# Kernel tuning notes

Measured on AMD Instinct MI355X. Metric: run time of the kernel, lower is better.

The kernel has to match this reference:

```python
import jax, jax.numpy as jnp
import numpy as np
from jax import lax

# Paraformer-large streaming decoder dims
L, H, DFF, NH, DK, K, V, T, S, CKV, LB = 16, 512, 2048, 4, 128, 11, 8404, 64, 2048, 256, 256


def _ln(x, g, b, eps=1e-5):
    m = jnp.mean(x, axis=-1, keepdims=True)
    var = jnp.mean((x - m) ** 2, axis=-1, keepdims=True)
    return (x - m) * lax.rsqrt(var + eps) * g + b


def setup_inputs() -> dict:
    key = jax.random.key(0)
    ks = jax.random.split(key, 20)
    w = lambda k, shp: jax.random.normal(k, shp, jnp.float32) * 0.02
    return {
        "encoder_out": jax.random.normal(ks[0], (1, S, H), jnp.float32),
        "list_frame": jax.random.normal(ks[1], (1, T, H), jnp.float32),
        "fsmn_cache": jax.random.normal(ks[2], (L, 1, H, K - 1), jnp.float32),
        "key_cache": jax.random.normal(ks[3], (L, NH, DK, CKV), jnp.float32),
        "value_cache": jax.random.normal(ks[4], (L, NH, CKV, DK), jnp.float32),
        "norm1_g": jnp.ones((L, H)), "norm1_b": jnp.zeros((L, H)),
        "norm2_g": jnp.ones((L, H)), "norm2_b": jnp.zeros((L, H)),
        "norm3_g": jnp.ones((L, H)), "norm3_b": jnp.zeros((L, H)),
        "ffn_norm_g": jnp.ones((L, DFF)), "ffn_norm_b": jnp.zeros((L, DFF)),
        "w1": w(ks[5], (L, H, DFF)), "b1": jnp.zeros((L, DFF)),
        "w2": w(ks[6], (L, DFF, H)),  # bias-free in FunASR DecoderSANM
        "fsmn_w": w(ks[7], (L, H, K)),  # depthwise conv, groups=H, no bias
        "qw": w(ks[8], (L, H, H)), "qb": jnp.zeros((L, H)),
        "kvw": w(ks[9], (L, H, 2 * H)), "kvb": jnp.zeros((L, 2 * H)),
        "ow": w(ks[10], (L, H, H)), "ob": jnp.zeros((L, H)),
        "d3_norm1_g": jnp.ones((H,)), "d3_norm1_b": jnp.zeros((H,)),
        "d3_w1": w(ks[11], (H, DFF)), "d3_b1": jnp.zeros((DFF,)),
        "d3_ffn_norm_g": jnp.ones((DFF,)), "d3_ffn_norm_b": jnp.zeros((DFF,)),
        "d3_w2": w(ks[12], (DFF, H)),
        "after_norm_g": jnp.ones((H,)), "after_norm_b": jnp.zeros((H,)),
        "out_w": w(ks[13], (H, V)), "out_b": jnp.zeros((V,)),
        "list_frame_len": T,
    }


def reference(encoder_out, list_frame, fsmn_cache, key_cache, value_cache,
              norm1_g, norm1_b, norm2_g, norm2_b, norm3_g, norm3_b,
              ffn_norm_g, ffn_norm_b, w1, b1, w2, fsmn_w, qw, qb, kvw, kvb, ow, ob,
              d3_norm1_g, d3_norm1_b, d3_w1, d3_b1, d3_ffn_norm_g, d3_ffn_norm_b, d3_w2,
              after_norm_g, after_norm_b, out_w, out_b, list_frame_len):
    enc = encoder_out[0]  # [S, H]
    scale = DK ** -0.5

    def layer_fn(lf, p):
        (fc, kc, vc, n1g, n1b, n2g, n2b, n3g, n3b, fng, fnb,
         W1, B1, W2, FW, QW, QB, KVW, KVB, OW, OB) = p
        residual = lf
        y = _ln(lf, n1g, n1b)
        y = _ln(jax.nn.relu(y @ W1 + B1), fng, fnb) @ W2
        y = _ln(y, n2g, n2b)
        # cache concat; slice [look_back:] with look_back = -(K-1)-T keeps all K-1+T cols
        x_cat = jnp.concatenate([fc, jnp.swapaxes(y, 1, 2)], axis=-1)  # [1, H, K-1+T]
        conv = lax.conv_general_dilated(
            x_cat, FW[:, None, :], (1,), 'VALID',
            dimension_numbers=('NCH', 'OIH', 'NCH'), feature_group_count=H)  # [1, H, T]
        x = jnp.swapaxes(conv, 1, 2) + y + residual
        residual = x
        q = (_ln(x, n3g, n3b)[0] @ QW + QB).reshape(-1, NH, DK).transpose(1, 0, 2) * scale  # [h, T, dk]
        kv = enc @ KVW + KVB  # [S, 2H]
        k = kv[:, :H].reshape(-1, NH, DK).transpose(1, 2, 0)  # [h, dk, S]
        v = kv[:, H:].reshape(-1, NH, DK).transpose(1, 0, 2)  # [h, S, dk]
        k = jnp.concatenate([kc, k], axis=2)  # [h, dk, CKV+S]
        v = jnp.concatenate([vc, v], axis=1)  # [h, CKV+S, dk]
        attn = jax.nn.softmax(jnp.einsum('htd,hds->hts', q, k), axis=-1)
        ctx = jnp.einsum('hts,hsd->htd', attn, v).transpose(1, 0, 2).reshape(1, -1, H)
        lf = residual + ctx @ OW + OB
        return lf, (x_cat, k[:, :, -LB:], v[:, -LB:, :])

    layer_params = (fsmn_cache, key_cache, value_cache, norm1_g, norm1_b, norm2_g, norm2_b,
                    norm3_g, norm3_b, ffn_norm_g, ffn_norm_b, w1, b1, w2, fsmn_w,
                    qw, qb, kvw, kvb, ow, ob)
    lf, (save_fsmn, save_keys, save_values) = lax.scan(layer_fn, list_frame, layer_params)
    x = _ln(lf, d3_norm1_g, d3_norm1_b)
    x = _ln(jax.nn.relu(x @ d3_w1 + d3_b1), d3_ffn_norm_g, d3_ffn_norm_b) @ d3_w2
    logits = _ln(x, after_norm_g, after_norm_b) @ out_w + out_b
    max_logit_ids = jnp.argmax(logits, axis=-1).astype(jnp.int32)
    return save_fsmn, save_keys, save_values, max_logit_ids
```

## Files before the change

### kernel.cpp

```cpp
#include <hip/hip_runtime.h>

constexpr int LAY = 16, HID = 512, FF = 2048, NHD = 4, DKH = 128, KW = 11,
              VOC = 8404, TT = 64, SEQ = 2048, LBN = 256;

__global__ void diag_k(float* __restrict__ p, float v) { p[threadIdx.x] = v; }

__global__ __launch_bounds__(256) void copy_k(const float* __restrict__ in,
                                              float* __restrict__ out, int n) {
  const int i = blockIdx.x * 256 + threadIdx.x;
  if (i < n) out[i] = in[i];
}

__global__ __launch_bounds__(256) void ln_k(const float* __restrict__ src,
                                            const float* __restrict__ g,
                                            const float* __restrict__ b,
                                            float* __restrict__ dst, int cols) {
  __shared__ float buf[2048];
  __shared__ float red[256];
  const int tid = threadIdx.x;
  const int row = blockIdx.x;
  src += (size_t)row * cols;
  dst += (size_t)row * cols;
  float s = 0.f;
  for (int c = tid; c < cols; c += 256) { float v = src[c]; buf[c] = v; s += v; }
  red[tid] = s; __syncthreads();
  for (int st = 128; st > 0; st >>= 1) { if (tid < st) red[tid] += red[tid + st]; __syncthreads(); }
  const float mean = red[0] / cols;
  __syncthreads();
  float vs = 0.f;
  for (int c = tid; c < cols; c += 256) { float d = buf[c] - mean; vs += d * d; }
  red[tid] = vs; __syncthreads();
  for (int st = 128; st > 0; st >>= 1) { if (tid < st) red[tid] += red[tid + st]; __syncthreads(); }
  const float inv = rsqrtf(red[0] / cols + 1e-5f);
  for (int c = tid; c < cols; c += 256) dst[c] = (buf[c] - mean) * inv * g[c] + b[c];
}

__global__ __launch_bounds__(256) void gemm_nn(
    const float* __restrict__ A, int lda, long sA,
    const float* __restrict__ B, int ldb, long sB,
    float* __restrict__ C, int ldc, long sC,
    const float* __restrict__ bias,
    const float* __restrict__ res, int ldres,
    int N, int Kd, int flags, int nch,
    float* __restrict__ part, long pzs, int coff) {
  __shared__ float As[64][68];
  __shared__ float Bs[64][68];
  const int tid = threadIdx.x;
  const int lr = tid >> 4, lc = tid & 15;
  const int bn = blockIdx.x * 64;
  const int chunk = blockIdx.y;
  const int z = blockIdx.z;
  A += (long)z * sA; B += (long)z * sB; C += (long)z * sC;
  float acc[4][4] = {};
  const int ktiles = Kd >> 6;
  for (int kt = chunk; kt < ktiles; kt += nch) {
    const int k0 = kt << 6;
    __syncthreads();
#pragma unroll
    for (int i = 0; i < 4; ++i) {
      const int r = lr + 16 * i;
      const float4 av = *(const float4*)(A + (size_t)r * lda + k0 + lc * 4);
      As[lc * 4 + 0][r] = av.x; As[lc * 4 + 1][r] = av.y;
      As[lc * 4 + 2][r] = av.z; As[lc * 4 + 3][r] = av.w;
      const int n = bn + lc * 4;
      const float* bp = B + (size_t)(k0 + r) * ldb + n;
      float4 bv;
      if (n + 3 < N) bv = *(const float4*)bp;
      else {
        bv.x = (n + 0 < N) ? bp[0] : 0.f;
        bv.y = (n + 1 < N) ? bp[1] : 0.f;
        bv.z = (n + 2 < N) ? bp[2] : 0.f;
        bv.w = (n + 3 < N) ? bp[3] : 0.f;
      }
      *(float4*)(&Bs[r][lc * 4]) = bv;
    }
    __syncthreads();
#pragma unroll 8
    for (int kk = 0; kk < 64; ++kk) {
      const float4 a = *(const float4*)(&As[kk][lr * 4]);
      const float4 b = *(const float4*)(&Bs[kk][lc * 4]);
      acc[0][0] += a.x * b.x; acc[0][1] += a.x * b.y; acc[0][2] += a.x * b.z; acc[0][3] += a.x * b.w;
      acc[1][0] += a.y * b.x; acc[1][1] += a.y * b.y; acc[1][2] += a.y * b.z; acc[1][3] += a.y * b.w;
      acc[2][0] += a.z * b.x; acc[2][1] += a.z * b.y; acc[2][2] += a.z * b.z; acc[2][3] += a.z * b.w;
      acc[3][0] += a.w * b.x; acc[3][1] += a.w * b.y; acc[3][2] += a.w * b.z; acc[3][3] += a.w * b.w;
    }
  }
  if (part) {
    float* P = part + (size_t)z * pzs + (size_t)(coff + chunk) * 64 * N;
#pragma unroll
    for (int i = 0; i < 4; ++i) {
      const int m = lr * 4 + i;
#pragma unroll
      for (int j = 0; j < 4; ++j) P[(size_t)m * N + bn + lc * 4 + j] = acc[i][j];
    }
    return;
  }
#pragma unroll
  for (int i = 0; i < 4; ++i) {
    const int m = lr * 4 + i;
#pragma unroll
    for (int j = 0; j < 4; ++j) {
      const int n = bn + lc * 4 + j;
      if (n < N) {
        float v = acc[i][j];
        if (bias) v += bias[n];
        if (res) v += res[(size_t)m * ldres + n];
        if (flags & 2) v += C[(size_t)m * ldc + n];
        if (flags & 1) v = fmaxf(v, 0.f);
        C[(size_t)m * ldc + n] = v;
      }
    }
  }
}

__global__ __launch_bounds__(256) void red_k(
    const float* __restrict__ P, float* __restrict__ out,
    int N, int nch, long pzs, int outld, int zoff,
    const float* __restrict__ bias, const float* __restrict__ res,
    const float* __restrict__ rsv, const float* __restrict__ bvv,
    int relu, int total) {
  const int idx = blockIdx.x * 256 + threadIdx.x;
  if (idx >= total) return;
  const int z = idx / (64 * N);
  const int rem = idx - z * 64 * N;
  const int t = rem / N;
  const int n = rem - t * N;
  const float* p = P + (size_t)z * pzs + (size_t)t * N + n;
  float s = 0.f;
  for (int c = 0; c < nch; ++c) s += p[(size_t)c * 64 * N];
  const int oc = z * zoff + n;
  if (bias) s += bias[oc];
  if (res) s += res[(size_t)t * outld + oc];
  if (rsv) s += rsv[z * 64 + t] * bvv[oc];
  if (relu) s = fmaxf(s, 0.f);
  out[(size_t)t * outld + oc] = s;
}

__global__ __launch_bounds__(256) void gemm_nt(
    const float* __restrict__ A, int lda, long sA,
    const float* __restrict__ B, int ldb, long sB,
    float* __restrict__ C, int ldc, long sC,
    int N, int Kd) {
  __shared__ float As[64][68];
  __shared__ float Bs[64][68];
  const int tid = threadIdx.x;
  const int lr = tid >> 4, lc = tid & 15;
  const int bn = blockIdx.x * 64;
  const int z = blockIdx.z;
  A += (long)z * sA; B += (long)z * sB; C += (long)z * sC;
  float acc[4][4] = {};
  for (int k0 = 0; k0 < Kd; k0 += 64) {
    __syncthreads();
#pragma unroll
    for (int i = 0; i < 4; ++i) {
      const int r = lr + 16 * i;
      const float4 av = *(const float4*)(A + (size_t)r * lda + k0 + lc * 4);
      As[lc * 4 + 0][r] = av.x; As[lc * 4 + 1][r] = av.y;
      As[lc * 4 + 2][r] = av.z; As[lc * 4 + 3][r] = av.w;
      const float4 bv = *(const float4*)(B + (size_t)(bn + r) * ldb + k0 + lc * 4);
      Bs[lc * 4 + 0][r] = bv.x; Bs[lc * 4 + 1][r] = bv.y;
      Bs[lc * 4 + 2][r] = bv.z; Bs[lc * 4 + 3][r] = bv.w;
    }
    __syncthreads();
#pragma unroll 8
    for (int kk = 0; kk < 64; ++kk) {
      const float4 a = *(const float4*)(&As[kk][lr * 4]);
      const float4 b = *(const float4*)(&Bs[kk][lc * 4]);
      acc[0][0] += a.x * b.x; acc[0][1] += a.x * b.y; acc[0][2] += a.x * b.z; acc[0][3] += a.x * b.w;
      acc[1][0] += a.y * b.x; acc[1][1] += a.y * b.y; acc[1][2] += a.y * b.z; acc[1][3] += a.y * b.w;
      acc[2][0] += a.z * b.x; acc[2][1] += a.z * b.y; acc[2][2] += a.z * b.z; acc[2][3] += a.z * b.w;
      acc[3][0] += a.w * b.x; acc[3][1] += a.w * b.y; acc[3][2] += a.w * b.z; acc[3][3] += a.w * b.w;
    }
  }
#pragma unroll
  for (int i = 0; i < 4; ++i) {
    const int m = lr * 4 + i;
#pragma unroll
    for (int j = 0; j < 4; ++j) {
      const int n = bn + lc * 4 + j;
      C[(size_t)m * ldc + n] = acc[i][j];
    }
  }
}

__global__ __launch_bounds__(128) void fsmn_k(const float* __restrict__ y4,
                                              const float* __restrict__ lfin,
                                              const float* __restrict__ cache,
                                              const float* __restrict__ fw,
                                              float* __restrict__ xout,
                                              float* __restrict__ xcat_out) {
  __shared__ float xc[KW - 1 + TT];
  const int tid = threadIdx.x, h = blockIdx.x;
  if (tid < KW - 1) xc[tid] = cache[h * (KW - 1) + tid];
  else if (tid < KW - 1 + TT) xc[tid] = y4[(size_t)(tid - (KW - 1)) * HID + h];
  __syncthreads();
  if (tid < KW - 1 + TT) xcat_out[h * (KW - 1 + TT) + tid] = xc[tid];
  if (tid < TT) {
    float a = 0.f;
#pragma unroll
    for (int k = 0; k < KW; ++k) a += xc[tid + k] * fw[h * KW + k];
    const size_t o = (size_t)tid * HID + h;
    xout[o] = a + y4[o] + lfin[o];
  }
}

__global__ __launch_bounds__(256) void qc_k(const float* __restrict__ qbf,
                                            const float* __restrict__ kb,
                                            float* __restrict__ qc) {
  const int tid = threadIdx.x;
  const int h = tid >> 6, t = tid & 63;
  float s = 0.f;
#pragma unroll 8
  for (int d = 0; d < DKH; ++d) s += qbf[t * HID + h * DKH + d] * kb[h * DKH + d];
  qc[tid] = s;
}

__global__ __launch_bounds__(256) void softmax_k(float* __restrict__ sc,
                                                 float* __restrict__ rs,
                                                 const float* __restrict__ qc,
                                                 int cols, int newStart, float alpha) {
  __shared__ float red[256];
  const int tid = threadIdx.x;
  const int row = blockIdx.x;
  sc += (size_t)row * cols;
  const float qcv = qc[row];
  float m = -3.4e38f;
  for (int c = tid; c < cols; c += 256) {
    float v = (sc[c] + (c >= newStart ? qcv : 0.f)) * alpha;
    m = fmaxf(m, v);
  }
  red[tid] = m; __syncthreads();
  for (int st = 128; st > 0; st >>= 1) { if (tid < st) red[tid] = fmaxf(red[tid], red[tid + st]); __syncthreads(); }
  m = red[0]; __syncthreads();
  float s = 0.f;
  for (int c = tid; c < cols; c += 256) {
    float v = (sc[c] + (c >= newStart ? qcv : 0.f)) * alpha;
    float e = __expf(v - m);
    sc[c] = e; s += e;
  }
  red[tid] = s; __syncthreads();
  for (int st = 128; st > 0; st >>= 1) { if (tid < st) red[tid] += red[tid + st]; __syncthreads(); }
  const float inv = 1.f / red[0];
  float ns = 0.f;
  for (int c = tid; c < cols; c += 256) {
    float p = sc[c] * inv; sc[c] = p;
    if (c >= newStart) ns += p;
  }
  __syncthreads();
  red[tid] = ns; __syncthreads();
  for (int st = 128; st > 0; st >>= 1) { if (tid < st) red[tid] += red[tid + st]; __syncthreads(); }
  if (tid == 0) rs[row] = red[0];
}

__global__ __launch_bounds__(256) void argmax_k(const float* __restrict__ lg,
                                                float* __restrict__ out) {
  __shared__ float vs[256];
  __shared__ int ix[256];
  const int tid = threadIdx.x;
  lg += (size_t)blockIdx.x * VOC;
  float bm = -3.4e38f;
  int bi = 0;
  for (int c = tid; c < VOC; c += 256) { float v = lg[c]; if (v > bm) { bm = v; bi = c; } }
  vs[tid] = bm; ix[tid] = bi; __syncthreads();
  for (int st = 128; st > 0; st >>= 1) {
    if (tid < st) {
      if (vs[tid + st] > vs[tid] || (vs[tid + st] == vs[tid] && ix[tid + st] < ix[tid])) {
        vs[tid] = vs[tid + st]; ix[tid] = ix[tid + st];
      }
    }
    __syncthreads();
  }
  if (tid == 0) out[blockIdx.x] = (float)ix[0];
}

__global__ __launch_bounds__(256) void kvsave_k(const float* __restrict__ enc,
                                                const float* __restrict__ kvw,
                                                const float* __restrict__ kvb,
                                                float* __restrict__ keys,
                                                float* __restrict__ vals) {
  __shared__ float As[64][68];
  __shared__ float Bs[64][68];
  const int tid = threadIdx.x;
  const int lr = tid >> 4, lc = tid & 15;
  const int bn = blockIdx.x * 64, bm = blockIdx.y * 64;
  const int l = blockIdx.z;
  const float* W = kvw + (size_t)l * HID * 2 * HID;
  float acc[4][4] = {};
  for (int k0 = 0; k0 < HID; k0 += 64) {
    __syncthreads();
#pragma unroll
    for (int i = 0; i < 4; ++i) {
      const int r = lr + 16 * i;
      const float4 av =
          *(const float4*)(enc + (size_t)(SEQ - LBN + bm + r) * HID + k0 + lc * 4);
      As[lc * 4 + 0][r] = av.x; As[lc * 4 + 1][r] = av.y;
      As[lc * 4 + 2][r] = av.z; As[lc * 4 + 3][r] = av.w;
      const float4 bv = *(const float4*)(W + (size_t)(k0 + r) * (2 * HID) + bn + lc * 4);
      *(float4*)(&Bs[r][lc * 4]) = bv;
    }
    __syncthreads();
#pragma unroll 8
    for (int kk = 0; kk < 64; ++kk) {
      const float4 a = *(const float4*)(&As[kk][lr * 4]);
      const float4 b = *(const float4*)(&Bs[kk][lc * 4]);
      acc[0][0] += a.x * b.x; acc[0][1] += a.x * b.y; acc[0][2] += a.x * b.z; acc[0][3] += a.x * b.w;
      acc[1][0] += a.y * b.x; acc[1][1] += a.y * b.y; acc[1][2] += a.y * b.z; acc[1][3] += a.y * b.w;
      acc[2][0] += a.z * b.x; acc[2][1] += a.z * b.y; acc[2][2] += a.z * b.z; acc[2][3] += a.z * b.w;
      acc[3][0] += a.w * b.x; acc[3][1] += a.w * b.y; acc[3][2] += a.w * b.z; acc[3][3] += a.w * b.w;
    }
  }
#pragma unroll
  for (int i = 0; i < 4; ++i) {
    const int m = bm + lr * 4 + i;
#pragma unroll
    for (int j = 0; j < 4; ++j) {
      const int n = bn + lc * 4 + j;
      const float v = acc[i][j] + kvb[(size_t)l * 2 * HID + n];
      if (n < 512) {
        const int h = n >> 7, d = n & 127;
        keys[(((size_t)l * NHD + h) * DKH + d) * LBN + m] = v;
      } else {
        const int c = n - 512, h = c >> 7, d = c & 127;
        vals[(((size_t)l * NHD + h) * LBN + m) * DKH + d] = v;
      }
    }
  }
}

extern "C" void kernel_launch(void* const* d_in, const int* in_sizes, int n_in,
                              void* d_out, int out_size, void* d_ws, size_t ws_size,
                              hipStream_t stream) {
  static const int EXPECT[34] = {
      1048576, 32768, 81920, -1, -1,
      8192, 8192, 8192, 8192, 8192, 8192,
      32768, 32768,
      16777216, 32768, 16777216, 90112,
      4194304, 8192, 8388608, 16384, 4194304, 8192,
      512, 512, 1048576, 2048, 2048, 2048, 1048576,
      512, 512, 4302848, 8404};
  if (out_size != 4800576) {
    diag_k<<<1, 64, 0, stream>>>((float*)d_out, 9800000.f);
    return;
  }
  float* out_fsmn = (float*)d_out;
  float* out_keys = out_fsmn + (size_t)LAY * HID * (KW - 1 + TT);
  float* out_vals = out_keys + (size_t)LAY * NHD * DKH * LBN;
  float* out_ids  = out_vals + (size_t)LAY * NHD * LBN * DKH;
  if (n_in < 34) {
    diag_k<<<1, 64, 0, stream>>>(out_ids, 9900000.f);
    return;
  }
  for (int i = 0; i < 34; ++i) {
    if (EXPECT[i] >= 0 && in_sizes[i] != EXPECT[i]) {
      diag_k<<<1, 64, 0, stream>>>(out_ids, (float)((i + 1) * 100000));
      return;
    }
  }
  const long per = (long)LAY * NHD * DKH;
  const long ckl = (long)in_sizes[3] / per;
  if ((long)in_sizes[3] != ckl * per || in_sizes[4] != in_sizes[3] ||
      ckl <= 0 || (ckl & 63) != 0 || ckl > 6144) {
    diag_k<<<1, 64, 0, stream>>>(out_fsmn, (float)in_sizes[3]);
    return;
  }
  const int ckv = (int)ckl;
  const int sct = ckv + SEQ;
  const long TS = (long)TT * sct;
  const int ncho = (ckv / 64 < 8) ? (ckv / 64) : 8;

  const float* enc    = (const float*)d_in[0];
  const float* lfrm   = (const float*)d_in[1];
  const float* fcache = (const float*)d_in[2];
  const float* kcache = (const float*)d_in[3];
  const float* vcache = (const float*)d_in[4];
  const float* n1g = (const float*)d_in[5];  const float* n1b = (const float*)d_in[6];
  const float* n2g = (const float*)d_in[7];  const float* n2b = (const float*)d_in[8];
  const float* n3g = (const float*)d_in[9];  const float* n3b = (const float*)d_in[10];
  const float* fng = (const float*)d_in[11]; const float* fnb = (const float*)d_in[12];
  const float* w1  = (const float*)d_in[13]; const float* b1  = (const float*)d_in[14];
  const float* w2  = (const float*)d_in[15];
  const float* fw  = (const float*)d_in[16];
  const float* qw  = (const float*)d_in[17]; const float* qbi  = (const float*)d_in[18];
  const float* kvw = (const float*)d_in[19]; const float* kvbi = (const float*)d_in[20];
  const float* ow  = (const float*)d_in[21]; const float* obi  = (const float*)d_in[22];
  const float* d3n1g = (const float*)d_in[23]; const float* d3n1b = (const float*)d_in[24];
  const float* d3w1  = (const float*)d_in[25]; const float* d3b1  = (const float*)d_in[26];
  const float* d3fng = (const float*)d_in[27]; const float* d3fnb = (const float*)d_in[28];
  const float* d3w2  = (const float*)d_in[29];
  const float* ang   = (const float*)d_in[30]; const float* anb = (const float*)d_in[31];
  const float* outw  = (const float*)d_in[32]; const float* outb = (const float*)d_in[33];

  float* sc  = out_keys;
  float* ov  = out_vals;
  float* lf  = ov + 0;
  float* y1  = ov + 32768;
  float* y3  = ov + 65536;
  float* y4  = ov + 98304;
  float* xb  = ov + 131072;
  float* qbf = ov + 163840;
  float* ctx = ov + 196608;
  float* h1  = ov + 229376;
  float* y2  = ov + 360448;
  float* qp  = ov + 491520;
  float* ce  = ov + 622592;
  float* qc  = ov + 753664;
  float* rs  = ov + 753920;
  float* lg  = ov + 754176;
  float* part= ov + 1292032;

  const float alpha = 0.08838834764831845f;
  const long TH = (long)TT * HID;
  const long pz_ctx = (long)(ncho + 4) * 64 * DKH;

  copy_k<<<128, 256, 0, stream>>>(lfrm, lf, TT * HID);

  for (int l = 0; l < LAY; ++l) {
    const float* Wkv = kvw + (size_t)l * HID * 2 * HID;
    const float* Bkv = kvbi + (size_t)l * 2 * HID;
    ln_k<<<TT, 256, 0, stream>>>(lf, n1g + l * HID, n1b + l * HID, y1, HID);
    gemm_nn<<<dim3(32, 4, 1), 256, 0, stream>>>(
        y1, HID, 0, w1 + (size_t)l * HID * FF, FF, 0, nullptr, 0, 0,
        nullptr, nullptr, 0, FF, HID, 0, 4, part, 4L * 64 * FF, 0);
    red_k<<<512, 256, 0, stream>>>(part, h1, FF, 4, 0, FF, FF,
                                   b1 + (size_t)l * FF, nullptr, nullptr, nullptr,
                                   1, TT * FF);
    ln_k<<<TT, 256, 0, stream>>>(h1, fng + (size_t)l * FF, fnb + (size_t)l * FF, y2, FF);
    gemm_nn<<<dim3(8, 16, 1), 256, 0, stream>>>(
        y2, FF, 0, w2 + (size_t)l * FF * HID, HID, 0, nullptr, 0, 0,
        nullptr, nullptr, 0, HID, FF, 0, 16, part, 16L * 64 * HID, 0);
    red_k<<<128, 256, 0, stream>>>(part, y3, HID, 16, 0, HID, HID,
                                   nullptr, nullptr, nullptr, nullptr, 0, TT * HID);
    ln_k<<<TT, 256, 0, stream>>>(y3, n2g + l * HID, n2b + l * HID, y4, HID);
    fsmn_k<<<HID, 128, 0, stream>>>(y4, lf, fcache + (size_t)l * HID * (KW - 1),
                                    fw + (size_t)l * HID * KW, xb,
                                    out_fsmn + (size_t)l * HID * (KW - 1 + TT));
    ln_k<<<TT, 256, 0, stream>>>(xb, n3g + l * HID, n3b + l * HID, y1, HID);
    gemm_nn<<<dim3(8, 8, 1), 256, 0, stream>>>(
        y1, HID, 0, qw + (size_t)l * HID * HID, HID, 0, nullptr, 0, 0,
        nullptr, nullptr, 0, HID, HID, 0, 8, part, 8L * 64 * HID, 0);
    red_k<<<128, 256, 0, stream>>>(part, qbf, HID, 8, 0, HID, HID,
                                   qbi + (size_t)l * HID, nullptr, nullptr, nullptr,
                                   0, TT * HID);
    gemm_nt<<<dim3(8, 1, NHD), 256, 0, stream>>>(
        qbf, HID, DKH, Wkv, 2 * HID, DKH, qp, HID, TH, HID, DKH);
    qc_k<<<1, 256, 0, stream>>>(qbf, Bkv, qc);
    gemm_nn<<<dim3(ckv / 64, 1, NHD), 256, 0, stream>>>(
        qbf, HID, DKH, kcache + (size_t)l * NHD * DKH * ckv, ckv, (long)DKH * ckv,
        sc, sct, TS, nullptr, nullptr, 0, ckv, DKH, 0, 1, nullptr, 0, 0);
    gemm_nt<<<dim3(32, 1, NHD), 256, 0, stream>>>(
        qp, HID, TH, enc, HID, 0, sc + ckv, sct, TS, SEQ, HID);
    softmax_k<<<NHD * TT, 256, 0, stream>>>(sc, rs, qc, sct, ckv, alpha);
    gemm_nn<<<dim3(2, ncho, NHD), 256, 0, stream>>>(
        sc, sct, TS, vcache + (size_t)l * NHD * ckv * DKH, DKH, (long)ckv * DKH,
        nullptr, 0, 0, nullptr, nullptr, 0, DKH, ckv, 0, ncho, part, pz_ctx, 0);
    gemm_nn<<<dim3(8, 4, NHD), 256, 0, stream>>>(
        sc + ckv, sct, TS, enc, HID, 0, nullptr, 0, 0,
        nullptr, nullptr, 0, HID, SEQ, 0, 4, part + 393216, 4L * 64 * HID, 0);
    red_k<<<512, 256, 0, stream>>>(part + 393216, ce, HID, 4, 4L * 64 * HID, HID, TH,
                                   nullptr, nullptr, nullptr, nullptr, 0, NHD * TT * HID);
    gemm_nn<<<dim3(2, 4, NHD), 256, 0, stream>>>(
        ce, HID, TH, Wkv + HID, 2 * HID, DKH, nullptr, 0, 0,
        nullptr, nullptr, 0, DKH, HID, 0, 4, part, pz_ctx, ncho);
    red_k<<<128, 256, 0, stream>>>(part, ctx, DKH, ncho + 4, pz_ctx, HID, DKH,
                                   nullptr, nullptr, rs, Bkv + HID, 0, NHD * TT * DKH);
    gemm_nn<<<dim3(8, 8, 1), 256, 0, stream>>>(
        ctx, HID, 0, ow + (size_t)l * HID * HID, HID, 0, nullptr, 0, 0,
        nullptr, nullptr, 0, HID, HID, 0, 8, part, 8L * 64 * HID, 0);
    red_k<<<128, 256, 0, stream>>>(part, lf, HID, 8, 0, HID, HID,
                                   obi + (size_t)l * HID, xb, nullptr, nullptr,
                                   0, TT * HID);
  }

  ln_k<<<TT, 256, 0, stream>>>(lf, d3n1g, d3n1b, y1, HID);
  gemm_nn<<<dim3(32, 4, 1), 256, 0, stream>>>(
      y1, HID, 0, d3w1, FF, 0, nullptr, 0, 0, nullptr, nullptr, 0,
      FF, HID, 0, 4, part, 4L * 64 * FF, 0);
  red_k<<<512, 256, 0, stream>>>(part, h1, FF, 4, 0, FF, FF,
                                 d3b1, nullptr, nullptr, nullptr, 1, TT * FF);
  ln_k<<<TT, 256, 0, stream>>>(h1, d3fng, d3fnb, y2, FF);
  gemm_nn<<<dim3(8, 16, 1), 256, 0, stream>>>(
      y2, FF, 0, d3w2, HID, 0, nullptr, 0, 0, nullptr, nullptr, 0,
      HID, FF, 0, 16, part, 16L * 64 * HID, 0);
  red_k<<<128, 256, 0, stream>>>(part, y3, HID, 16, 0, HID, HID,
                                 nullptr, nullptr, nullptr, nullptr, 0, TT * HID);
  ln_k<<<TT, 256, 0, stream>>>(y3, ang, anb, y4, HID);
  gemm_nn<<<dim3((VOC + 63) / 64, 1, 1), 256, 0, stream>>>(
      y4, HID, 0, outw, VOC, 0, lg, VOC, 0, outb, nullptr, 0,
      VOC, HID, 0, 1, nullptr, 0, 0);
  argmax_k<<<TT, 256, 0, stream>>>(lg, out_ids);

  kvsave_k<<<dim3(2 * HID / 64, LBN / 64, LAY), 256, 0, stream>>>(
      enc, kvw, kvbi, out_keys, out_vals);
}
```

Measured before the change: 3.123 ms.

## Fuse split-K reductions into layernorm and merge attention GEMM launches

Replaces the separate split-K reduction and layernorm kernels with one redln_k that sums partials, adds bias/residual/relu and normalises in a single pass. It merges the qp and cache-score GEMMs into attn1_k and the two context GEMMs into attn2_k, and folds the qc dot product into softmax. The ce reduction is dropped by summing split-K partials while loading the A tile of the following GEMM. The aim is to cut kernel launches and intermediate global round-trips per layer. In exchange, LN now runs on only 64 blocks and partial sums are re-read inside GEMM tile loads.

```diff
diff --git a/kernel.cpp b/kernel.cpp
--- a/kernel.cpp
+++ b/kernel.cpp
@@ -5,34 +5,36 @@
 
 __global__ void diag_k(float* __restrict__ p, float v) { p[threadIdx.x] = v; }
 
-__global__ __launch_bounds__(256) void copy_k(const float* __restrict__ in,
-                                              float* __restrict__ out, int n) {
-  const int i = blockIdx.x * 256 + threadIdx.x;
-  if (i < n) out[i] = in[i];
-}
-
-__global__ __launch_bounds__(256) void ln_k(const float* __restrict__ src,
-                                            const float* __restrict__ g,
-                                            const float* __restrict__ b,
-                                            float* __restrict__ dst, int cols) {
+__global__ __launch_bounds__(256) void redln_k(
+    const float* __restrict__ P, int N, int nch,
+    const float* __restrict__ bias, const float* __restrict__ res, int relu,
+    const float* __restrict__ g, const float* __restrict__ b,
+    float* __restrict__ out1, float* __restrict__ out2) {
   __shared__ float buf[2048];
   __shared__ float red[256];
-  const int tid = threadIdx.x;
-  const int row = blockIdx.x;
-  src += (size_t)row * cols;
-  dst += (size_t)row * cols;
+  const int m = blockIdx.x, tid = threadIdx.x;
   float s = 0.f;
-  for (int c = tid; c < cols; c += 256) { float v = src[c]; buf[c] = v; s += v; }
+  for (int n = tid; n < N; n += 256) {
+    const float* p = P + (size_t)m * N + n;
+    float v = 0.f;
+    for (int c = 0; c < nch; ++c) v += p[(size_t)c * 64 * N];
+    if (bias) v += bias[n];
+    if (res) v += res[(size_t)m * N + n];
+    if (relu) v = fmaxf(v, 0.f);
+    if (out1) out1[(size_t)m * N + n] = v;
+    buf[n] = v; s += v;
+  }
   red[tid] = s; __syncthreads();
   for (int st = 128; st > 0; st >>= 1) { if (tid < st) red[tid] += red[tid + st]; __syncthreads(); }
-  const float mean = red[0] / cols;
+  const float mean = red[0] / N;
   __syncthreads();
   float vs = 0.f;
-  for (int c = tid; c < cols; c += 256) { float d = buf[c] - mean; vs += d * d; }
+  for (int n = tid; n < N; n += 256) { float d = buf[n] - mean; vs += d * d; }
   red[tid] = vs; __syncthreads();
   for (int st = 128; st > 0; st >>= 1) { if (tid < st) red[tid] += red[tid + st]; __syncthreads(); }
-  const float inv = rsqrtf(red[0] / cols + 1e-5f);
-  for (int c = tid; c < cols; c += 256) dst[c] = (buf[c] - mean) * inv * g[c] + b[c];
+  const float inv = rsqrtf(red[0] / N + 1e-5f);
+  for (int n = tid; n < N; n += 256)
+    out2[(size_t)m * N + n] = (buf[n] - mean) * inv * g[n] + b[n];
 }
 
 __global__ __launch_bounds__(256) void gemm_nn(
@@ -42,7 +44,8 @@
     const float* __restrict__ bias,
     const float* __restrict__ res, int ldres,
     int N, int Kd, int flags, int nch,
-    float* __restrict__ part, long pzs, int coff) {
+    float* __restrict__ part, long pzs, int coff,
+    int aCh, long aChS) {
   __shared__ float As[64][68];
   __shared__ float Bs[64][68];
   const int tid = threadIdx.x;
@@ -59,7 +62,12 @@
 #pragma unroll
     for (int i = 0; i < 4; ++i) {
       const int r = lr + 16 * i;
-      const float4 av = *(const float4*)(A + (size_t)r * lda + k0 + lc * 4);
+      const float* ap = A + (size_t)r * lda + k0 + lc * 4;
+      float4 av = *(const float4*)ap;
+      for (int c = 1; c < aCh; ++c) {
+        const float4 t2 = *(const float4*)(ap + (size_t)c * aChS);
+        av.x += t2.x; av.y += t2.y; av.z += t2.z; av.w += t2.w;
+      }
       As[lc * 4 + 0][r] = av.x; As[lc * 4 + 1][r] = av.y;
       As[lc * 4 + 2][r] = av.z; As[lc * 4 + 3][r] = av.w;
       const int n = bn + lc * 4;
@@ -183,6 +191,125 @@
   }
 }
 
+__global__ __launch_bounds__(256) void attn1_k(
+    const float* __restrict__ qbf, const float* __restrict__ Wkv,
+    const float* __restrict__ kcl,
+    float* __restrict__ qp, float* __restrict__ sc,
+    int ckv, int sct) {
+  __shared__ float As[64][68];
+  __shared__ float Bs[64][68];
+  const int tid = threadIdx.x;
+  const int lr = tid >> 4, lc = tid & 15;
+  const int h = blockIdx.z;
+  const bool isQp = blockIdx.x < 8;
+  const int bn = (isQp ? blockIdx.x : blockIdx.x - 8) * 64;
+  const float* A = qbf + h * DKH;
+  float acc[4][4] = {};
+  for (int k0 = 0; k0 < DKH; k0 += 64) {
+    __syncthreads();
+#pragma unroll
+    for (int i = 0; i < 4; ++i) {
+      const int r = lr + 16 * i;
+      const float4 av = *(const float4*)(A + (size_t)r * HID + k0 + lc * 4);
+      As[lc * 4 + 0][r] = av.x; As[lc * 4 + 1][r] = av.y;
+      As[lc * 4 + 2][r] = av.z; As[lc * 4 + 3][r] = av.w;
+      if (isQp) {
+        const float4 bv = *(const float4*)(Wkv + (size_t)(bn + r) * (2 * HID) + h * DKH + k0 + lc * 4);
+        Bs[lc * 4 + 0][r] = bv.x; Bs[lc * 4 + 1][r] = bv.y;
+        Bs[lc * 4 + 2][r] = bv.z; Bs[lc * 4 + 3][r] = bv.w;
+      } else {
+        const float4 bv = *(const float4*)(kcl + ((size_t)h * DKH + k0 + r) * ckv + bn + lc * 4);
+        *(float4*)(&Bs[r][lc * 4]) = bv;
+      }
+    }
+    __syncthreads();
+#pragma unroll 8
+    for (int kk = 0; kk < 64; ++kk) {
+      const float4 a = *(const float4*)(&As[kk][lr * 4]);
+      const float4 b = *(const float4*)(&Bs[kk][lc * 4]);
+      acc[0][0] += a.x * b.x; acc[0][1] += a.x * b.y; acc[0][2] += a.x * b.z; acc[0][3] += a.x * b.w;
+      acc[1][0] += a.y * b.x; acc[1][1] += a.y * b.y; acc[1][2] += a.y * b.z; acc[1][3] += a.y * b.w;
+      acc[2][0] += a.z * b.x; acc[2][1] += a.z * b.y; acc[2][2] += a.z * b.z; acc[2][3] += a.z * b.w;
+      acc[3][0] += a.w * b.x; acc[3][1] += a.w * b.y; acc[3][2] += a.w * b.z; acc[3][3] += a.w * b.w;
+    }
+  }
+  if (isQp) {
+    float* C = qp + (size_t)h * TT * HID;
+#pragma unroll
+    for (int i = 0; i < 4; ++i)
+#pragma unroll
+      for (int j = 0; j < 4; ++j)
+        C[(size_t)(lr * 4 + i) * HID + bn + lc * 4 + j] = acc[i][j];
+  } else {
+    float* C = sc + (size_t)h * TT * sct;
+#pragma unroll
+    for (int i = 0; i < 4; ++i)
+#pragma unroll
+      for (int j = 0; j < 4; ++j)
+        C[(size_t)(lr * 4 + i) * sct + bn + lc * 4 + j] = acc[i][j];
+  }
+}
+
+__global__ __launch_bounds__(256) void attn2_k(
+    const float* __restrict__ sc, const float* __restrict__ vcl,
+    const float* __restrict__ enc,
+    float* __restrict__ part, float* __restrict__ partE,
+    int ckv, int sct, int ncho, long pzc) {
+  __shared__ float As[64][68];
+  __shared__ float Bs[64][68];
+  const int tid = threadIdx.x;
+  const int lr = tid >> 4, lc = tid & 15;
+  const int h = blockIdx.z;
+  const int by = blockIdx.y;
+  const bool isOld = blockIdx.x < 2;
+  if (isOld && by >= ncho) return;
+  if (!isOld && by >= 4) return;
+  const float* A;
+  const float* Bb;
+  int lda, ldb, N, ktiles, nch, bn;
+  float* P;
+  if (isOld) {
+    A = sc + (size_t)h * TT * sct;  lda = sct;
+    Bb = vcl + (size_t)h * ckv * DKH; ldb = DKH;
+    N = DKH; ktiles = ckv >> 6; nch = ncho; bn = blockIdx.x * 64;
+    P = part + (size_t)h * pzc + (size_t)by * 64 * DKH;
+  } else {
+    A = sc + ckv + (size_t)h * TT * sct; lda = sct;
+    Bb = enc; ldb = HID;
+    N = HID; ktiles = SEQ >> 6; nch = 4; bn = (blockIdx.x - 2) * 64;
+    P = partE + (size_t)h * (4L * 64 * HID) + (size_t)by * 64 * HID;
+  }
+  float acc[4][4] = {};
+  for (int kt = by; kt < ktiles; kt += nch) {
+    const int k0 = kt << 6;
+    __syncthreads();
+#pragma unroll
+    for (int i = 0; i < 4; ++i) {
+      const int r = lr + 16 * i;
+      const float4 av = *(const float4*)(A + (size_t)r * lda + k0 + lc * 4);
+      As[lc * 4 + 0][r] = av.x; As[lc * 4 + 1][r] = av.y;
+      As[lc * 4 + 2][r] = av.z; As[lc * 4 + 3][r] = av.w;
+      const float4 bv = *(const float4*)(Bb + (size_t)(k0 + r) * ldb + bn + lc * 4);
+      *(float4*)(&Bs[r][lc * 4]) = bv;
+    }
+    __syncthreads();
+#pragma unroll 8
+    for (int kk = 0; kk < 64; ++kk) {
+      const float4 a = *(const float4*)(&As[kk][lr * 4]);
+      const float4 b = *(const float4*)(&Bs[kk][lc * 4]);
+      acc[0][0] += a.x * b.x; acc[0][1] += a.x * b.y; acc[0][2] += a.x * b.z; acc[0][3] += a.x * b.w;
+      acc[1][0] += a.y * b.x; acc[1][1] += a.y * b.y; acc[1][2] += a.y * b.z; acc[1][3] += a.y * b.w;
+      acc[2][0] += a.z * b.x; acc[2][1] += a.z * b.y; acc[2][2] += a.z * b.z; acc[2][3] += a.z * b.w;
+      acc[3][0] += a.w * b.x; acc[3][1] += a.w * b.y; acc[3][2] += a.w * b.z; acc[3][3] += a.w * b.w;
+    }
+  }
+#pragma unroll
+  for (int i = 0; i < 4; ++i)
+#pragma unroll
+    for (int j = 0; j < 4; ++j)
+      P[(size_t)(lr * 4 + i) * N + bn + lc * 4 + j] = acc[i][j];
+}
+
 __global__ __launch_bounds__(128) void fsmn_k(const float* __restrict__ y4,
                                               const float* __restrict__ lfin,
                                               const float* __restrict__ cache,
@@ -204,26 +331,22 @@
   }
 }
 
-__global__ __launch_bounds__(256) void qc_k(const float* __restrict__ qbf,
-                                            const float* __restrict__ kb,
-                                            float* __restrict__ qc) {
-  const int tid = threadIdx.x;
-  const int h = tid >> 6, t = tid & 63;
-  float s = 0.f;
-#pragma unroll 8
-  for (int d = 0; d < DKH; ++d) s += qbf[t * HID + h * DKH + d] * kb[h * DKH + d];
-  qc[tid] = s;
-}
-
 __global__ __launch_bounds__(256) void softmax_k(float* __restrict__ sc,
                                                  float* __restrict__ rs,
-                                                 const float* __restrict__ qc,
+                                                 const float* __restrict__ qbf,
+                                                 const float* __restrict__ kb,
                                                  int cols, int newStart, float alpha) {
   __shared__ float red[256];
   const int tid = threadIdx.x;
   const int row = blockIdx.x;
+  const int h = row >> 6, t = row & 63;
   sc += (size_t)row * cols;
-  const float qcv = qc[row];
+  float qv = 0.f;
+  if (tid < DKH) qv = qbf[t * HID + h * DKH + tid] * kb[h * DKH + tid];
+  red[tid] = qv; __syncthreads();
+  for (int st = 64; st > 0; st >>= 1) { if (tid < st) red[tid] += red[tid + st]; __syncthreads(); }
+  const float qcv = red[0];
+  __syncthreads();
   float m = -3.4e38f;
   for (int c = tid; c < cols; c += 256) {
     float v = (sc[c] + (c >= newStart ? qcv : 0.f)) * alpha;
@@ -394,99 +517,84 @@
   float* ov  = out_vals;
   float* lf  = ov + 0;
   float* y1  = ov + 32768;
-  float* y3  = ov + 65536;
   float* y4  = ov + 98304;
   float* xb  = ov + 131072;
   float* qbf = ov + 163840;
   float* ctx = ov + 196608;
-  float* h1  = ov + 229376;
   float* y2  = ov + 360448;
   float* qp  = ov + 491520;
-  float* ce  = ov + 622592;
-  float* qc  = ov + 753664;
   float* rs  = ov + 753920;
   float* lg  = ov + 754176;
-  float* part= ov + 1292032;
+  float* partE = lg;
+  float* part  = ov + 1292032;
 
   const float alpha = 0.08838834764831845f;
   const long TH = (long)TT * HID;
   const long pz_ctx = (long)(ncho + 4) * 64 * DKH;
 
-  copy_k<<<128, 256, 0, stream>>>(lfrm, lf, TT * HID);
+  redln_k<<<TT, 256, 0, stream>>>(lfrm, HID, 1, nullptr, nullptr, 0,
+                                  n1g, n1b, lf, y1);
 
   for (int l = 0; l < LAY; ++l) {
     const float* Wkv = kvw + (size_t)l * HID * 2 * HID;
     const float* Bkv = kvbi + (size_t)l * 2 * HID;
-    ln_k<<<TT, 256, 0, stream>>>(lf, n1g + l * HID, n1b + l * HID, y1, HID);
     gemm_nn<<<dim3(32, 4, 1), 256, 0, stream>>>(
         y1, HID, 0, w1 + (size_t)l * HID * FF, FF, 0, nullptr, 0, 0,
-        nullptr, nullptr, 0, FF, HID, 0, 4, part, 4L * 64 * FF, 0);
-    red_k<<<512, 256, 0, stream>>>(part, h1, FF, 4, 0, FF, FF,
-                                   b1 + (size_t)l * FF, nullptr, nullptr, nullptr,
-                                   1, TT * FF);
-    ln_k<<<TT, 256, 0, stream>>>(h1, fng + (size_t)l * FF, fnb + (size_t)l * FF, y2, FF);
+        nullptr, nullptr, 0, FF, HID, 0, 4, part, 0, 0, 1, 0);
+    redln_k<<<TT, 256, 0, stream>>>(part, FF, 4, b1 + (size_t)l * FF, nullptr, 1,
+                                    fng + (size_t)l * FF, fnb + (size_t)l * FF,
+                                    nullptr, y2);
     gemm_nn<<<dim3(8, 16, 1), 256, 0, stream>>>(
         y2, FF, 0, w2 + (size_t)l * FF * HID, HID, 0, nullptr, 0, 0,
-        nullptr, nullptr, 0, HID, FF, 0, 16, part, 16L * 64 * HID, 0);
-    red_k<<<128, 256, 0, stream>>>(part, y3, HID, 16, 0, HID, HID,
-                                   nullptr, nullptr, nullptr, nullptr, 0, TT * HID);
-    ln_k<<<TT, 256, 0, stream>>>(y3, n2g + l * HID, n2b + l * HID, y4, HID);
+        nullptr, nullptr, 0, HID, FF, 0, 16, part, 0, 0, 1, 0);
+    redln_k<<<TT, 256, 0, stream>>>(part, HID, 16, nullptr, nullptr, 0,
+                                    n2g + l * HID, n2b + l * HID, nullptr, y4);
     fsmn_k<<<HID, 128, 0, stream>>>(y4, lf, fcache + (size_t)l * HID * (KW - 1),
                                     fw + (size_t)l * HID * KW, xb,
                                     out_fsmn + (size_t)l * HID * (KW - 1 + TT));
-    ln_k<<<TT, 256, 0, stream>>>(xb, n3g + l * HID, n3b + l * HID, y1, HID);
+    redln_k<<<TT, 256, 0, stream>>>(xb, HID, 1, nullptr, nullptr, 0,
+                                    n3g + l * HID, n3b + l * HID, nullptr, y1);
     gemm_nn<<<dim3(8, 8, 1), 256, 0, stream>>>(
         y1, HID, 0, qw + (size_t)l * HID * HID, HID, 0, nullptr, 0, 0,
-        nullptr, nullptr, 0, HID, HID, 0, 8, part, 8L * 64 * HID, 0);
+        nullptr, nullptr, 0, HID, HID, 0, 8, part, 0, 0, 1, 0);
     red_k<<<128, 256, 0, stream>>>(part, qbf, HID, 8, 0, HID, HID,
                                    qbi + (size_t)l * HID, nullptr, nullptr, nullptr,
                                    0, TT * HID);
-    gemm_nt<<<dim3(8, 1, NHD), 256, 0, stream>>>(
-        qbf, HID, DKH, Wkv, 2 * HID, DKH, qp, HID, TH, HID, DKH);
-    qc_k<<<1, 256, 0, stream>>>(qbf, Bkv, qc);
-    gemm_nn<<<dim3(ckv / 64, 1, NHD), 256, 0, stream>>>(
-        qbf, HID, DKH, kcache + (size_t)l * NHD * DKH * ckv, ckv, (long)DKH * ckv,
-        sc, sct, TS, nullptr, nullptr, 0, ckv, DKH, 0, 1, nullptr, 0, 0);
+    attn1_k<<<dim3(8 + ckv / 64, 1, NHD), 256, 0, stream>>>(
+        qbf, Wkv, kcache + (size_t)l * NHD * DKH * ckv, qp, sc, ckv, sct);
     gemm_nt<<<dim3(32, 1, NHD), 256, 0, stream>>>(
         qp, HID, TH, enc, HID, 0, sc + ckv, sct, TS, SEQ, HID);
-    softmax_k<<<NHD * TT, 256, 0, stream>>>(sc, rs, qc, sct, ckv, alpha);
-    gemm_nn<<<dim3(2, ncho, NHD), 256, 0, stream>>>(
-        sc, sct, TS, vcache + (size_t)l * NHD * ckv * DKH, DKH, (long)ckv * DKH,
-        nullptr, 0, 0, nullptr, nullptr, 0, DKH, ckv, 0, ncho, part, pz_ctx, 0);
-    gemm_nn<<<dim3(8, 4, NHD), 256, 0, stream>>>(
-        sc + ckv, sct, TS, enc, HID, 0, nullptr, 0, 0,
-        nullptr, nullptr, 0, HID, SEQ, 0, 4, part + 393216, 4L * 64 * HID, 0);
-    red_k<<<512, 256, 0, stream>>>(part + 393216, ce, HID, 4, 4L * 64 * HID, HID, TH,
-                                   nullptr, nullptr, nullptr, nullptr, 0, NHD * TT * HID);
+    softmax_k<<<NHD * TT, 256, 0, stream>>>(sc, rs, qbf, Bkv, sct, ckv, alpha);
+    attn2_k<<<dim3(10, (ncho > 4 ? ncho : 4), NHD), 256, 0, stream>>>(
+        sc, vcache + (size_t)l * NHD * ckv * DKH, enc, part, partE,
+        ckv, sct, ncho, pz_ctx);
     gemm_nn<<<dim3(2, 4, NHD), 256, 0, stream>>>(
-        ce, HID, TH, Wkv + HID, 2 * HID, DKH, nullptr, 0, 0,
-        nullptr, nullptr, 0, DKH, HID, 0, 4, part, pz_ctx, ncho);
+        partE, HID, 4L * 64 * HID, Wkv + HID, 2 * HID, DKH, nullptr, 0, 0,
+        nullptr, nullptr, 0, DKH, HID, 0, 4, part, pz_ctx, ncho, 4, 64L * HID);
     red_k<<<128, 256, 0, stream>>>(part, ctx, DKH, ncho + 4, pz_ctx, HID, DKH,
                                    nullptr, nullptr, rs, Bkv + HID, 0, NHD * TT * DKH);
     gemm_nn<<<dim3(8, 8, 1), 256, 0, stream>>>(
         ctx, HID, 0, ow + (size_t)l * HID * HID, HID, 0, nullptr, 0, 0,
-        nullptr, nullptr, 0, HID, HID, 0, 8, part, 8L * 64 * HID, 0);
-    red_k<<<128, 256, 0, stream>>>(part, lf, HID, 8, 0, HID, HID,
-                                   obi + (size_t)l * HID, xb, nullptr, nullptr,
-                                   0, TT * HID);
-  }
-
-  ln_k<<<TT, 256, 0, stream>>>(lf, d3n1g, d3n1b, y1, HID);
+        nullptr, nullptr, 0, HID, HID, 0, 8, part, 0, 0, 1, 0);
+    const float* ng = (l + 1 < LAY) ? n1g + (l + 1) * HID : d3n1g;
+    const float* nb = (l + 1 < LAY) ? n1b + (l + 1) * HID : d3n1b;
+    redln_k<<<TT, 256, 0, stream>>>(part, HID, 8, obi + (size_t)l * HID, xb, 0,
+                                    ng, nb, lf, y1);
+  }
+
   gemm_nn<<<dim3(32, 4, 1), 256, 0, stream>>>(
       y1, HID, 0, d3w1, FF, 0, nullptr, 0, 0, nullptr, nullptr, 0,
-      FF, HID, 0, 4, part, 4L * 64 * FF, 0);
-  red_k<<<512, 256, 0, stream>>>(part, h1, FF, 4, 0, FF, FF,
-                                 d3b1, nullptr, nullptr, nullptr, 1, TT * FF);
-  ln_k<<<TT, 256, 0, stream>>>(h1, d3fng, d3fnb, y2, FF);
+      FF, HID, 0, 4, part, 0, 0, 1, 0);
+  redln_k<<<TT, 256, 0, stream>>>(part, FF, 4, d3b1, nullptr, 1,
+                                  d3fng, d3fnb, nullptr, y2);
   gemm_nn<<<dim3(8, 16, 1), 256, 0, stream>>>(
       y2, FF, 0, d3w2, HID, 0, nullptr, 0, 0, nullptr, nullptr, 0,
-      HID, FF, 0, 16, part, 16L * 64 * HID, 0);
-  red_k<<<128, 256, 0, stream>>>(part, y3, HID, 16, 0, HID, HID,
-                                 nullptr, nullptr, nullptr, nullptr, 0, TT * HID);
-  ln_k<<<TT, 256, 0, stream>>>(y3, ang, anb, y4, HID);
+      HID, FF, 0, 16, part, 0, 0, 1, 0);
+  redln_k<<<TT, 256, 0, stream>>>(part, HID, 16, nullptr, nullptr, 0,
+                                  ang, anb, nullptr, y4);
   gemm_nn<<<dim3((VOC + 63) / 64, 1, 1), 256, 0, stream>>>(
       y4, HID, 0, outw, VOC, 0, lg, VOC, 0, outb, nullptr, 0,
-      VOC, HID, 0, 1, nullptr, 0, 0);
+      VOC, HID, 0, 1, nullptr, 0, 0, 1, 0);
   argmax_k<<<TT, 256, 0, stream>>>(lg, out_ids);
 
   kvsave_k<<<dim3(2 * HID / 64, LBN / 64, LAY), 256, 0, stream>>>(
```

Result: faster. 2.985 ms (-4.4%).
